# Performance work log

Measured on AMD Instinct MI355X. Metric: run time of the kernel, lower is better.

## Reference

```python
import jax, jax.numpy as jnp
import numpy as np
from jax import lax

DIM = 256
POS = 32
RATIO = 4
LN_EPS = 1e-5


def _layernorm(x, g, b):
    m = x.mean(-1, keepdims=True)
    v = ((x - m) ** 2).mean(-1, keepdims=True)
    return (x - m) * lax.rsqrt(v + LN_EPS) * g + b


def _pos_embed(pos, h, w):
    # pos: [1, C, POS, POS] -> bilinear (align_corners=False / half-pixel) -> [1, h*w, C]
    p = jax.image.resize(pos, (1, pos.shape[1], h, w), method='bilinear')
    return p.transpose(0, 2, 3, 1).reshape(1, h * w, pos.shape[1])


def _scan_branch(u, ln_g, ln_b, Wf, bf, Ww, bw, Wo, bo):
    # u: [B, N, C]. Pooled LN context -> concat gates -> gated linear recurrence.
    c = _layernorm(u.mean(1), ln_g, ln_b)                       # [B, C]
    z = jnp.concatenate([u, jnp.broadcast_to(c[:, None, :], u.shape)], -1)
    d = jax.nn.softplus(z @ Wf + bf)
    g = jax.nn.sigmoid(z @ Ww + bw)
    o = jax.nn.sigmoid(z @ Wo + bo)
    a = jnp.exp(-d)
    b = (1.0 - a) * (g * u)

    def step(s, t):
        a_t, b_t, o_t, u_t = t
        s = a_t * s + b_t
        return s, o_t * s + (1.0 - o_t) * u_t

    xs = tuple(jnp.swapaxes(v, 0, 1) for v in (a, b, o, u))     # [N, B, C]
    s0 = jnp.zeros((u.shape[0], u.shape[2]), u.dtype)
    _, y = lax.scan(step, s0, xs)
    return jnp.swapaxes(y, 0, 1)                                # [B, N, C]


def setup_inputs() -> dict:
    key = jax.random.key(0)
    ks = jax.random.split(key, 32)
    d = DIM

    def W(k, i, o, s=0.02):
        return (jax.random.normal(k, (i, o), jnp.float32) * s)

    inp = {
        'x': jax.random.normal(ks[0], (8, d, 64, 64), jnp.float32),
        'Wt': W(ks[1], d, d), 'bt': jnp.zeros((d,), jnp.float32),
        'pos_fine': jax.random.normal(ks[2], (1, d, POS, POS), jnp.float32) * 0.02,
        'pos_glob': jax.random.normal(ks[3], (1, d, POS, POS), jnp.float32) * 0.02,
        'ln_g': jnp.ones((d,), jnp.float32), 'ln_b': jnp.zeros((d,), jnp.float32),
        'Wf': W(ks[4], 2 * d, d), 'bf': jnp.zeros((d,), jnp.float32),
        'Ww': W(ks[5], 2 * d, d), 'bw': jnp.zeros((d,), jnp.float32),
        'Wo': W(ks[6], 2 * d, d), 'bo': jnp.zeros((d,), jnp.float32),
        'Wr': W(ks[7], 3 * d, d), 'br': jnp.zeros((d,), jnp.float32),
        'Wgi': W(ks[8], 3 * d, d), 'bgi': jnp.zeros((d,), jnp.float32),
        'dw_w': jax.random.normal(ks[9], (d, 1, 3, 3), jnp.float32) * 0.1,
        'dw_b': jnp.zeros((d,), jnp.float32),
        'Wl': W(ks[10], d, d), 'bl': jnp.zeros((d,), jnp.float32),
        'Wlf': W(ks[11], 2 * d, d), 'blf': jnp.zeros((d,), jnp.float32),
        'Wout': W(ks[12], d, d), 'bout': jnp.zeros((d,), jnp.float32),
    }
    return inp


def reference(x, Wt, bt, pos_fine, pos_glob, ln_g, ln_b, Wf, bf, Ww, bw, Wo, bo,
              Wr, br, Wgi, bgi, dw_w, dw_b, Wl, bl, Wlf, blf, Wout, bout):
    bsz, c, h, w = x.shape
    gate_params = (ln_g, ln_b, Wf, bf, Ww, bw, Wo, bo)

    # fine sequence: token proj + interpolated learnable pos
    seq = x.transpose(0, 2, 3, 1).reshape(bsz, h * w, c)
    u = seq @ Wt + bt + _pos_embed(pos_fine, h, w)

    # bidirectional gated scan
    y_f = _scan_branch(u, *gate_params)
    y_b = jnp.flip(_scan_branch(jnp.flip(u, 1), *gate_params), 1)
    rho = jax.nn.sigmoid(jnp.concatenate([u, y_f, y_b], -1) @ Wr + br)
    y = rho * y_f + (1.0 - rho) * y_b

    # global branch: exact avg pool (H,W divisible by RATIO) -> scan -> upsample
    gh, gw = h // RATIO, w // RATIO
    x_g = x.reshape(bsz, c, gh, RATIO, gw, RATIO).mean((3, 5))
    seq_g = x_g.transpose(0, 2, 3, 1).reshape(bsz, gh * gw, c)
    u_g = seq_g @ Wt + bt + _pos_embed(pos_glob, gh, gw)
    y_g = _scan_branch(u_g, *gate_params)
    y_g_map = y_g.reshape(bsz, gh, gw, c).transpose(0, 3, 1, 2)
    y_g_up = jax.image.resize(y_g_map, (bsz, c, h, w), method='bilinear')
    y_g_seq = y_g_up.transpose(0, 2, 3, 1).reshape(bsz, h * w, c)

    lam = jax.nn.sigmoid(jnp.concatenate([y, y_g_seq, u], -1) @ Wgi + bgi)
    z = y + lam * y_g_seq

    # local depthwise conv branch
    v_map = lax.conv_general_dilated(x, dw_w, (1, 1), 'SAME',
                                     feature_group_count=c) + dw_b[None, :, None, None]
    v = v_map.transpose(0, 2, 3, 1).reshape(bsz, h * w, c) @ Wl + bl
    eta = jax.nn.sigmoid(jnp.concatenate([v, z], -1) @ Wlf + blf)
    u_out = eta * v + (1.0 - eta) * z

    # 1x1 conv output proj + residual
    out_map = (u_out @ Wout + bout).reshape(bsz, h, w, c).transpose(0, 3, 1, 2)
    return x + out_map
```

## Files before the change

### kernel.cpp

```cpp
#include <hip/hip_runtime.h>
#include <cstddef>

#define B_  8
#define C_  256
#define H_  64
#define W_  64
#define HW_ 4096
#define NG_ 256

typedef unsigned short u16;
typedef __attribute__((ext_vector_type(8))) short short8;
typedef __attribute__((ext_vector_type(4))) float f32x4;

__device__ __forceinline__ float sigm(float v) { return 1.f / (1.f + expf(-v)); }

__device__ __forceinline__ u16 f2bf(float f) {
    union { float f; unsigned u; } x; x.f = f;
    unsigned r = x.u + 0x7fff + ((x.u >> 16) & 1);
    return (u16)(r >> 16);
}
__device__ __forceinline__ float bf2f(u16 h) {
    union { unsigned u; float f; } x; x.u = ((unsigned)h) << 16;
    return x.f;
}

__global__ __launch_bounds__(256) void prepw_k(
    const float* __restrict__ Wt, const float* __restrict__ Wf, const float* __restrict__ Ww,
    const float* __restrict__ Wo, const float* __restrict__ Wr, const float* __restrict__ Wgi,
    const float* __restrict__ Wl, const float* __restrict__ Wlf, const float* __restrict__ Wout,
    u16* __restrict__ Wpre)
{
    int s = blockIdx.z;
    const float* Wsrc; int rowoff = 0;
    switch (s) {
        case 0: Wsrc = Wt; break;
        case 1: Wsrc = Wf; break;
        case 2: Wsrc = Ww; break;
        case 3: Wsrc = Wo; break;
        case 4: case 5: case 6: Wsrc = Wr;  rowoff = (s - 4) * 256; break;
        case 7: case 8: case 9: Wsrc = Wgi; rowoff = (s - 7) * 256; break;
        case 10: Wsrc = Wl; break;
        case 11: case 12: Wsrc = Wlf; rowoff = (s - 11) * 256; break;
        default: Wsrc = Wout; break;
    }
    __shared__ float t[32][33];
    int k0 = blockIdx.y * 32, n0 = blockIdx.x * 32;
    int tx = threadIdx.x, ty = threadIdx.y;
#pragma unroll
    for (int i = 0; i < 32; i += 8)
        t[ty + i][tx] = Wsrc[(size_t)(rowoff + k0 + ty + i) * 256 + n0 + tx];
    __syncthreads();
    u16* op = Wpre + (size_t)s * 65536;
#pragma unroll
    for (int i = 0; i < 32; i += 8)
        op[(size_t)(n0 + ty + i) * 256 + k0 + tx] = f2bf(t[tx][ty + i]);
}

#define LDK 72
__global__ __launch_bounds__(256, 4) void gemm_bf16(
    const u16* __restrict__ A0, const u16* __restrict__ A1, const u16* __restrict__ A2,
    int nseg, const u16* __restrict__ Wpre, const float* __restrict__ bias,
    const float* __restrict__ pos, const float* __restrict__ aux0,
    const u16* __restrict__ auxb0, const u16* __restrict__ auxb1,
    float* __restrict__ out, u16* __restrict__ out2, int NTOK, int mode)
{
    __shared__ u16 Asm[64 * LDK];
    __shared__ u16 Bsm[128 * LDK];
    const int tid = threadIdx.x;
    const int lane = tid & 63, wave = tid >> 6;
    const int wm = wave & 1, wn = wave >> 1;
    const int m0 = blockIdx.x * 64, n0 = blockIdx.y * 128;
    const int l15 = lane & 15, lq = lane >> 4;

    f32x4 acc[2][4] = {};

    const int rowA = tid >> 2, kA = (tid & 3) * 16;
    const int rowB = tid >> 1, kB = (tid & 1) * 32;

    for (int seg = 0; seg < nseg; ++seg) {
        const u16* __restrict__ A = (seg == 0) ? A0 : ((seg == 1) ? A1 : A2);
        const u16* arow = A + (size_t)(m0 + rowA) * 256 + kA;
        const u16* wrow = Wpre + (size_t)seg * 65536 + (size_t)(n0 + rowB) * 256 + kB;

        for (int k0 = 0; k0 < 256; k0 += 64) {
            *(short8*)(&Asm[rowA * LDK + kA])     = *(const short8*)(arow + k0);
            *(short8*)(&Asm[rowA * LDK + kA + 8]) = *(const short8*)(arow + k0 + 8);
#pragma unroll
            for (int c = 0; c < 4; ++c)
                *(short8*)(&Bsm[rowB * LDK + kB + c * 8]) =
                    *(const short8*)(wrow + k0 + c * 8);
            __syncthreads();

#pragma unroll
            for (int ks = 0; ks < 2; ++ks) {
                short8 af[2], bfr[4];
#pragma unroll
                for (int i = 0; i < 2; ++i)
                    af[i] = *(const short8*)(&Asm[(wm * 32 + i * 16 + l15) * LDK + ks * 32 + lq * 8]);
#pragma unroll
                for (int j = 0; j < 4; ++j)
                    bfr[j] = *(const short8*)(&Bsm[(wn * 64 + j * 16 + l15) * LDK + ks * 32 + lq * 8]);
#pragma unroll
                for (int i = 0; i < 2; ++i)
#pragma unroll
                    for (int j = 0; j < 4; ++j)
                        acc[i][j] = __builtin_amdgcn_mfma_f32_16x16x32_bf16(
                            af[i], bfr[j], acc[i][j], 0, 0, 0);
            }
            __syncthreads();
        }
    }

#pragma unroll
    for (int i = 0; i < 2; ++i) {
        int mbase = m0 + wm * 32 + i * 16 + lq * 4;
#pragma unroll
        for (int j = 0; j < 4; ++j) {
            int n = n0 + wn * 64 + j * 16 + l15;
            if (mode == 9) {
                int b9 = mbase >> 12, hw = mbase & 4095;
                size_t oi = ((size_t)b9 * 256 + n) * 4096 + hw;
                float bn = bias[n];
                float4 xr = *(const float4*)(aux0 + oi);
                float4 res;
                res.x = xr.x + acc[i][j][0] + bn;
                res.y = xr.y + acc[i][j][1] + bn;
                res.z = xr.z + acc[i][j][2] + bn;
                res.w = xr.w + acc[i][j][3] + bn;
                *(float4*)(out + oi) = res;
                continue;
            }
            float bn = bias[n];
#pragma unroll
            for (int r = 0; r < 4; ++r) {
                int m = mbase + r;
                size_t idx = (size_t)m * 256 + n;
                float D = acc[i][j][r] + bn;
                if (mode == 1) {
                    float v = D + pos[(size_t)(m % NTOK) * 256 + n];
                    out[idx] = v; out2[idx] = f2bf(v);
                } else if (mode == 10) {
                    float v = D + pos[(size_t)(m % NTOK) * 256 + n];
                    out2[idx] = f2bf(v);
                } else if (mode == 11) {
                    float r_ = sigm(D);
                    out2[idx] = f2bf(r_ * bf2f(auxb0[idx]) + (1.f - r_) * bf2f(auxb1[idx]));
                } else if (mode == 6) {
                    float l = sigm(D);
                    out2[idx] = f2bf(bf2f(auxb1[idx]) + l * bf2f(auxb0[idx]));
                } else if (mode == 7) {
                    out2[idx] = f2bf(D);
                } else {
                    float e = sigm(D);
                    out2[idx] = f2bf(e * bf2f(auxb0[idx]) + (1.f - e) * bf2f(auxb1[idx]));
                }
            }
        }
    }
}

__global__ __launch_bounds__(256, 4) void gemm_gates3(
    const u16* __restrict__ A0, const u16* __restrict__ Wg, const float* __restrict__ cf,
    const u16* __restrict__ ubf, float* __restrict__ aF, float* __restrict__ bbF,
    u16* __restrict__ obf, int NTOK)
{
    __shared__ u16 Asm[64 * LDK];
    __shared__ u16 Bsm[3][64 * LDK];
    const int tid = threadIdx.x;
    const int lane = tid & 63, wave = tid >> 6;
    const int wm = wave & 1, wn = wave >> 1;
    const int m0 = blockIdx.x * 64, n0 = blockIdx.y * 64;
    const int l15 = lane & 15, lq = lane >> 4;

    f32x4 acc[3][2][2] = {};

    const int rowA = tid >> 2, kA = (tid & 3) * 16;
    const u16* arow = A0 + (size_t)(m0 + rowA) * 256 + kA;
    const u16* wrow = Wg + (size_t)(n0 + rowA) * 256 + kA;

    for (int k0 = 0; k0 < 256; k0 += 64) {
        *(short8*)(&Asm[rowA * LDK + kA])     = *(const short8*)(arow + k0);
        *(short8*)(&Asm[rowA * LDK + kA + 8]) = *(const short8*)(arow + k0 + 8);
#pragma unroll
        for (int ws = 0; ws < 3; ++ws) {
            const u16* wr = wrow + (size_t)ws * 65536 + k0;
            *(short8*)(&Bsm[ws][rowA * LDK + kA])     = *(const short8*)(wr);
            *(short8*)(&Bsm[ws][rowA * LDK + kA + 8]) = *(const short8*)(wr + 8);
        }
        __syncthreads();
#pragma unroll
        for (int ks = 0; ks < 2; ++ks) {
            short8 af[2];
#pragma unroll
            for (int i = 0; i < 2; ++i)
                af[i] = *(const short8*)(&Asm[(wm * 32 + i * 16 + l15) * LDK + ks * 32 + lq * 8]);
#pragma unroll
            for (int ws = 0; ws < 3; ++ws) {
                short8 bfr[2];
#pragma unroll
                for (int j = 0; j < 2; ++j)
                    bfr[j] = *(const short8*)(&Bsm[ws][(wn * 32 + j * 16 + l15) * LDK + ks * 32 + lq * 8]);
#pragma unroll
                for (int i = 0; i < 2; ++i)
#pragma unroll
                    for (int j = 0; j < 2; ++j)
                        acc[ws][i][j] = __builtin_amdgcn_mfma_f32_16x16x32_bf16(
                            af[i], bfr[j], acc[ws][i][j], 0, 0, 0);
            }
        }
        __syncthreads();
    }

#pragma unroll
    for (int i = 0; i < 2; ++i) {
        int mbase = m0 + wm * 32 + i * 16 + lq * 4;
        int bt_ = mbase / NTOK;
#pragma unroll
        for (int j = 0; j < 2; ++j) {
            int n = n0 + wn * 32 + j * 16 + l15;
            float cD = cf[((size_t)0 * B_ + bt_) * C_ + n];
            float cW = cf[((size_t)1 * B_ + bt_) * C_ + n];
            float cO = cf[((size_t)2 * B_ + bt_) * C_ + n];
#pragma unroll
            for (int r = 0; r < 4; ++r) {
                size_t idx = (size_t)(mbase + r) * 256 + n;
                float a_ = sigm(-(acc[0][i][j][r] + cD));
                float g_ = sigm(acc[1][i][j][r] + cW);
                float o_ = sigm(acc[2][i][j][r] + cO);
                float u_ = bf2f(ubf[idx]);
                aF[idx]  = a_;
                bbF[idx] = (1.f - a_) * g_ * u_;
                obf[idx] = f2bf(o_);
            }
        }
    }
}

__global__ __launch_bounds__(256) void transpose_bf_k(const float* __restrict__ in,
                                                      u16* __restrict__ outb)
{
    __shared__ float t[32][33];
    int b = blockIdx.z;
    int r0 = blockIdx.y * 32, c0 = blockIdx.x * 32;
    int tx = threadIdx.x, ty = threadIdx.y;
    const float* ip = in + (size_t)b * HW_ * C_;
    u16* op = outb + (size_t)b * HW_ * C_;
#pragma unroll
    for (int k = 0; k < 32; k += 8)
        t[ty + k][tx] = ip[(size_t)(r0 + ty + k) * HW_ + c0 + tx];
    __syncthreads();
#pragma unroll
    for (int k = 0; k < 32; k += 8)
        op[(size_t)(c0 + ty + k) * C_ + r0 + tx] = f2bf(t[tx][ty + k]);
}

__global__ __launch_bounds__(256) void dwconvt3_k(const float* __restrict__ x,
                                                  const float* __restrict__ dww,
                                                  const float* __restrict__ dwb,
                                                  u16* __restrict__ vseq)
{
    __shared__ float sx[32 * 384];
    __shared__ float sw[32 * 9];
    __shared__ float sb[32];
    const int t = threadIdx.x;
    const int l   = (blockIdx.x & 7) * 128 + (blockIdx.x >> 3);
    const int hch = l & 15;
    const int chb = (l >> 4) & 7;
    const int b   = l >> 7;
    const int r0 = chb * 32, h0 = hch * 4;

    for (int p = t; p < 288; p += 256) sw[p] = dww[(size_t)(r0 + p / 9) * 9 + p % 9];
    if (t < 32) sb[t] = dwb[r0 + t];

    const float* xb = x + (size_t)(b * 256 + r0) * 4096;
#pragma unroll
    for (int j = 0; j < 12; ++j) {
        int seg = j * 256 + t;
        int ch  = seg / 96;
        int r4  = seg - ch * 96;
        int rr  = r4 >> 4;
        int w4  = (r4 & 15) * 4;
        int hh  = h0 - 1 + rr;
        float4 v = make_float4(0.f, 0.f, 0.f, 0.f);
        if (hh >= 0 && hh <= 63)
            v = *(const float4*)(xb + (size_t)ch * 4096 + hh * 64 + w4);
        *(float4*)(&sx[seg * 4]) = v;
    }
    __syncthreads();

    const int w = t & 63, chq = t >> 6;
    float res[4][8];
#pragma unroll
    for (int i = 0; i < 8; ++i) {
        const int ch = chq * 8 + i;
        const float* cw = &sw[ch * 9];
        const float* bp = &sx[ch * 384 + w];
        float aa[4];
        aa[0] = aa[1] = aa[2] = aa[3] = sb[ch];
#pragma unroll
        for (int rr = 0; rr < 6; ++rr) {
            const float* rp = bp + rr * 64;
            float cc = rp[0];
            float lf = (w > 0)  ? rp[-1] : 0.f;
            float rt = (w < 63) ? rp[1]  : 0.f;
            if (rr < 4)            aa[rr]     += lf * cw[0] + cc * cw[1] + rt * cw[2];
            if (rr >= 1 && rr < 5) aa[rr - 1] += lf * cw[3] + cc * cw[4] + rt * cw[5];
            if (rr >= 2)           aa[rr - 2] += lf * cw[6] + cc * cw[7] + rt * cw[8];
        }
#pragma unroll
        for (int r = 0; r < 4; ++r) res[r][i] = aa[r];
    }

    size_t obase = ((size_t)b * HW_ + (size_t)(h0 * 64 + w)) * 256 + r0 + chq * 8;
#pragma unroll
    for (int r = 0; r < 4; ++r) {
        short8 v;
#pragma unroll
        for (int i = 0; i < 8; ++i) v[i] = (short)f2bf(res[r][i]);
        *(short8*)(vseq + obase + (size_t)r * 64 * 256) = v;
    }
}

__global__ __launch_bounds__(256) void pool_k(const float* __restrict__ x, u16* __restrict__ seqg)
{
    int b = blockIdx.x, c = blockIdx.y, ghw = threadIdx.x;
    int gh = ghw >> 4, gw = ghw & 15;
    const float* xp = x + ((size_t)b * C_ + c) * HW_;
    float s = 0.f;
#pragma unroll
    for (int dy = 0; dy < 4; ++dy)
#pragma unroll
        for (int dx = 0; dx < 4; ++dx)
            s += xp[(gh * 4 + dy) * W_ + gw * 4 + dx];
    seqg[((size_t)b * NG_ + ghw) * C_ + c] = f2bf(s * (1.f / 16.f));
}

__global__ __launch_bounds__(256) void posfine_k(const float* __restrict__ pf, float* __restrict__ posF)
{
    int hw = blockIdx.x, c = threadIdx.x;
    int h = hw >> 6, w = hw & 63;
    float fy = h * 0.5f - 0.25f, fx = w * 0.5f - 0.25f;
    int y0 = (int)floorf(fy); float wy = fy - (float)y0;
    int x0 = (int)floorf(fx); float wx = fx - (float)x0;
    int y0c = min(max(y0, 0), 31), y1c = min(max(y0 + 1, 0), 31);
    int x0c = min(max(x0, 0), 31), x1c = min(max(x0 + 1, 0), 31);
    const float* p = pf + (size_t)c * 1024;
    float v = (1.f - wy) * ((1.f - wx) * p[y0c * 32 + x0c] + wx * p[y0c * 32 + x1c])
            +        wy  * ((1.f - wx) * p[y1c * 32 + x0c] + wx * p[y1c * 32 + x1c]);
    posF[(size_t)hw * C_ + c] = v;
}

__global__ __launch_bounds__(256) void posglob_k(const float* __restrict__ pg, float* __restrict__ posG)
{
    int ghw = blockIdx.x, c = threadIdx.x;
    int gh = ghw >> 4, gw = ghw & 15;
    const float wt[4] = {0.125f, 0.375f, 0.375f, 0.125f};
    float wy[4], wx[4]; int jy[4], jx[4];
    float sy = 0.f, sx = 0.f;
#pragma unroll
    for (int k = 0; k < 4; ++k) {
        jy[k] = 2 * gh - 1 + k; jx[k] = 2 * gw - 1 + k;
        wy[k] = (jy[k] >= 0 && jy[k] < 32) ? wt[k] : 0.f; sy += wy[k];
        wx[k] = (jx[k] >= 0 && jx[k] < 32) ? wt[k] : 0.f; sx += wx[k];
    }
    const float* p = pg + (size_t)c * 1024;
    float acc = 0.f;
#pragma unroll
    for (int ky = 0; ky < 4; ++ky) {
        if (wy[ky] == 0.f) continue;
        float row = 0.f;
#pragma unroll
        for (int kx = 0; kx < 4; ++kx)
            if (wx[kx] != 0.f) row += wx[kx] * p[jy[ky] * 32 + jx[kx]];
        acc += wy[ky] * row;
    }
    posG[(size_t)ghw * C_ + c] = acc / (sy * sx);
}

__global__ __launch_bounds__(256) void upsample_k(const float* __restrict__ yg, u16* __restrict__ ygs)
{
    int b = blockIdx.x >> 12, hw = blockIdx.x & 4095, c = threadIdx.x;
    int h = hw >> 6, w = hw & 63;
    float fy = h * 0.25f - 0.375f, fx = w * 0.25f - 0.375f;
    int y0 = (int)floorf(fy); float wy = fy - (float)y0;
    int x0 = (int)floorf(fx); float wx = fx - (float)x0;
    int y0c = min(max(y0, 0), 15), y1c = min(max(y0 + 1, 0), 15);
    int x0c = min(max(x0, 0), 15), x1c = min(max(x0 + 1, 0), 15);
    const float* p = yg + (size_t)b * NG_ * C_ + c;
    float v = (1.f - wy) * ((1.f - wx) * p[(y0c * 16 + x0c) * C_] + wx * p[(y0c * 16 + x1c) * C_])
            +        wy  * ((1.f - wx) * p[(y1c * 16 + x0c) * C_] + wx * p[(y1c * 16 + x1c) * C_]);
    ygs[((size_t)b * HW_ + hw) * C_ + c] = f2bf(v);
}

__global__ __launch_bounds__(256) void meanpart_k(const float* __restrict__ u, float* __restrict__ part,
                                                  int Ntok, int chunkLen)
{
    int b = blockIdx.x, s = blockIdx.y, c = threadIdx.x;
    float acc = 0.f;
    for (int i = 0; i < chunkLen; ++i) {
        int t = s * chunkLen + i;
        acc += u[((size_t)b * Ntok + t) * C_ + c];
    }
    part[((size_t)b * gridDim.y + s) * C_ + c] = acc;
}

__global__ __launch_bounds__(256) void meanpart_bf_k(const u16* __restrict__ u, float* __restrict__ part,
                                                     int Ntok, int chunkLen)
{
    int b = blockIdx.x, s = blockIdx.y, c = threadIdx.x;
    float acc = 0.f;
    for (int i = 0; i < chunkLen; ++i) {
        int t = s * chunkLen + i;
        acc += bf2f(u[((size_t)b * Ntok + t) * C_ + c]);
    }
    part[((size_t)b * gridDim.y + s) * C_ + c] = acc;
}

__global__ __launch_bounds__(256) void ln_k(const float* __restrict__ part, int S, float invN,
                                            const float* __restrict__ g, const float* __restrict__ bta,
                                            float* __restrict__ cout)
{
    __shared__ float red[256];
    int c = threadIdx.x, b = blockIdx.x;
    float v = 0.f;
    for (int s = 0; s < S; ++s) v += part[((size_t)b * S + s) * C_ + c];
    v *= invN;
    red[c] = v; __syncthreads();
    for (int st = 128; st > 0; st >>= 1) { if (c < st) red[c] += red[c + st]; __syncthreads(); }
    float m = red[0] * (1.f / 256.f);
    __syncthreads();
    float d = v - m;
    red[c] = d * d; __syncthreads();
    for (int st = 128; st > 0; st >>= 1) { if (c < st) red[c] += red[c + st]; __syncthreads(); }
    float var = red[0] * (1.f / 256.f);
    cout[(size_t)b * C_ + c] = d * rsqrtf(var + 1e-5f) * g[c] + bta[c];
}

__global__ __launch_bounds__(256) void gatebias_k(const float* __restrict__ cvec,
    const float* __restrict__ Wf, const float* __restrict__ bf,
    const float* __restrict__ Ww, const float* __restrict__ bw,
    const float* __restrict__ Wo, const float* __restrict__ bo,
    float* __restrict__ outb)
{
    int n = threadIdx.x, b = blockIdx.x, gate = blockIdx.y;
    const float* Wm = (gate == 0) ? Wf : ((gate == 1) ? Ww : Wo);
    const float* bi = (gate == 0) ? bf : ((gate == 1) ? bw : bo);
    __shared__ float cs[256];
    cs[n] = cvec[(size_t)b * C_ + n];
    __syncthreads();
    float acc = bi[n];
    for (int k = 0; k < 256; ++k)
        acc += cs[k] * Wm[(size_t)(256 + k) * C_ + n];
    outb[((size_t)gate * B_ + b) * C_ + n] = acc;
}

__global__ __launch_bounds__(256) void scan_p1b(
    const float* __restrict__ a, const float* __restrict__ bb,
    float* __restrict__ AbF, float* __restrict__ BbF,
    float* __restrict__ AbB, float* __restrict__ BbB,
    int Ntok, int nchunk, int both)
{
    int c = threadIdx.x;
    int ch = blockIdx.x % nchunk;
    int b = blockIdx.x / nchunk;
    int CL = Ntok / nchunk;
    size_t base = ((size_t)b * Ntok + (size_t)ch * CL) * C_ + c;
    float sA = 1.f, sB = 0.f;
    for (int i = 0; i < CL; ++i) {
        float av = a[base + (size_t)i * C_];
        sB = av * sB + bb[base + (size_t)i * C_];
        sA *= av;
    }
    size_t o = ((size_t)b * nchunk + ch) * C_ + c;
    AbF[o] = sA; BbF[o] = sB;
    if (both) {
        sA = 1.f; sB = 0.f;
        for (int i = CL - 1; i >= 0; --i) {
            float av = a[base + (size_t)i * C_];
            sB = av * sB + bb[base + (size_t)i * C_];
            sA *= av;
        }
        size_t ob = ((size_t)b * nchunk + (nchunk - 1 - ch)) * C_ + c;
        AbB[ob] = sA; BbB[ob] = sB;
    }
}

__global__ __launch_bounds__(512) void scan_p2c(
    const float* __restrict__ AbF, const float* __restrict__ BbF, float* __restrict__ SbF,
    const float* __restrict__ AbB, const float* __restrict__ BbB, float* __restrict__ SbB,
    int nchunk, int both)
{
    const int c = threadIdx.x & 255, half = threadIdx.x >> 8, b = blockIdx.x;
    if (half && !both) return;
    const float* __restrict__ Ap = half ? AbB : AbF;
    const float* __restrict__ Bp = half ? BbB : BbF;
    float* __restrict__       Sp = half ? SbB : SbF;
    const size_t base = (size_t)b * nchunk * C_ + c;
    float a0[8], b0[8], a1[8], b1[8];
#pragma unroll
    for (int j = 0; j < 8; ++j) {
        a0[j] = Ap[base + (size_t)j * C_];
        b0[j] = Bp[base + (size_t)j * C_];
    }
    float s = 0.f;
    const int nb = nchunk >> 3;
    for (int t = 0; t < nb; ++t) {
        const size_t nbase = base + (size_t)(t + 1) * 8 * C_;
        if (t + 1 < nb) {
#pragma unroll
            for (int j = 0; j < 8; ++j) {
                a1[j] = Ap[nbase + (size_t)j * C_];
                b1[j] = Bp[nbase + (size_t)j * C_];
            }
        }
        const size_t cbase = base + (size_t)t * 8 * C_;
#pragma unroll
        for (int j = 0; j < 8; ++j) {
            Sp[cbase + (size_t)j * C_] = s;
            s = a0[j] * s + b0[j];
        }
#pragma unroll
        for (int j = 0; j < 8; ++j) { a0[j] = a1[j]; b0[j] = b1[j]; }
    }
}

__global__ __launch_bounds__(256) void scan_p3b(
    const float* __restrict__ a, const float* __restrict__ bb,
    const u16* __restrict__ obf, const u16* __restrict__ ubf,
    const float* __restrict__ SbF, const float* __restrict__ SbB,
    float* __restrict__ yout, u16* __restrict__ ybfF, u16* __restrict__ ybfB,
    int Ntok, int nchunk, int both)
{
    int c = threadIdx.x;
    int ch = blockIdx.x % nchunk;
    int b = blockIdx.x / nchunk;
    int CL = Ntok / nchunk;
    size_t base = ((size_t)b * Ntok + (size_t)ch * CL) * C_ + c;
    float s = SbF[((size_t)b * nchunk + ch) * C_ + c];
    for (int i = 0; i < CL; ++i) {
        size_t idx = base + (size_t)i * C_;
        float av = a[idx];
        s = av * s + bb[idx];
        float ov = bf2f(obf[idx]);
        float y = ov * s + (1.f - ov) * bf2f(ubf[idx]);
        if (yout) yout[idx] = y;
        if (ybfF) ybfF[idx] = f2bf(y);
    }
    if (both) {
        float sb = SbB[((size_t)b * nchunk + (nchunk - 1 - ch)) * C_ + c];
        for (int i = CL - 1; i >= 0; --i) {
            size_t idx = base + (size_t)i * C_;
            float av = a[idx];
            sb = av * sb + bb[idx];
            float ov = bf2f(obf[idx]);
            ybfB[idx] = f2bf(ov * sb + (1.f - ov) * bf2f(ubf[idx]));
        }
    }
}

extern "C" void kernel_launch(void* const* d_in, const int* in_sizes, int n_in,
                              void* d_out, int out_size, void* d_ws, size_t ws_size,
                              hipStream_t stream)
{
    const float* x        = (const float*)d_in[0];
    const float* Wt       = (const float*)d_in[1];
    const float* bt       = (const float*)d_in[2];
    const float* pos_fine = (const float*)d_in[3];
    const float* pos_glob = (const float*)d_in[4];
    const float* ln_g     = (const float*)d_in[5];
    const float* ln_b     = (const float*)d_in[6];
    const float* Wf       = (const float*)d_in[7];
    const float* bf       = (const float*)d_in[8];
    const float* Ww       = (const float*)d_in[9];
    const float* bw       = (const float*)d_in[10];
    const float* Wo       = (const float*)d_in[11];
    const float* bo       = (const float*)d_in[12];
    const float* Wr       = (const float*)d_in[13];
    const float* br       = (const float*)d_in[14];
    const float* Wgi      = (const float*)d_in[15];
    const float* bgi      = (const float*)d_in[16];
    const float* dww      = (const float*)d_in[17];
    const float* dwb      = (const float*)d_in[18];
    const float* Wl       = (const float*)d_in[19];
    const float* bl       = (const float*)d_in[20];
    const float* Wlf      = (const float*)d_in[21];
    const float* blf      = (const float*)d_in[22];
    const float* Wout     = (const float*)d_in[23];
    const float* bout     = (const float*)d_in[24];
    float* out = (float*)d_out;

    float* w = (float*)d_ws;
    const size_t BNC = (size_t)B_ * HW_ * C_;
    float* bu  = w + 0 * BNC;
    float* ba  = w + 1 * BNC;
    float* bbb = w + 2 * BNC;
    float* bo_ = w + 3 * BNC;
    u16* bf1 = (u16*)(w + 4 * BNC);
    u16* bf2 = bf1 + BNC;
    u16* bf3 = bf2 + BNC;
    u16* bf4 = bf3 + BNC;
    u16* bf5 = bf4 + BNC;
    float* ext = w + 4 * BNC + 5 * (BNC / 2);
    float* posF = ext;  ext += (size_t)HW_ * C_;
    float* posG = ext;  ext += (size_t)NG_ * C_;
    float* part = ext;  ext += (size_t)B_ * 32 * C_;
    float* cln  = ext;  ext += (size_t)B_ * C_;
    float* cf   = ext;  ext += (size_t)3 * B_ * C_;
    float* ug   = ext;  ext += (size_t)B_ * NG_ * C_;
    float* ag   = ext;  ext += (size_t)B_ * NG_ * C_;
    float* bbg  = ext;  ext += (size_t)B_ * NG_ * C_;
    float* ygt  = ext;  ext += (size_t)B_ * NG_ * C_;
    u16* seqg_bf = (u16*)ext;  ext += (size_t)B_ * NG_ * C_ / 2;
    u16* ug_bf   = (u16*)ext;  ext += (size_t)B_ * NG_ * C_ / 2;
    u16* og_bf   = (u16*)ext;  ext += (size_t)B_ * NG_ * C_ / 2;
    u16* Wpre    = (u16*)ext;
    const size_t CHS = (size_t)B_ * 256 * C_;
    float* chAF = bu + 0 * CHS;
    float* chBF = bu + 1 * CHS;
    float* chSF = bu + 2 * CHS;
    float* chAB = bu + 3 * CHS;
    float* chBB = bu + 4 * CHS;
    float* chSB = bu + 5 * CHS;
    u16* obf    = (u16*)bo_;

    const dim3 blk256(256);
    const dim3 blkT(32, 8);
    const dim3 gBig(B_ * HW_ / 64, 2);
    const dim3 gSml(B_ * NG_ / 64, 2);
    const dim3 gGateF(B_ * HW_ / 64, 4);
    const dim3 gGateG(B_ * NG_ / 64, 4);
    const size_t WS = 65536;
    const int NCH_F = 256;
    const int NCH_G = 16;
    const float *F0 = nullptr; const u16 *U0 = nullptr;
    float *FW = nullptr; u16 *UW = nullptr;

    prepw_k<<<dim3(8, 8, 14), blkT, 0, stream>>>(Wt, Wf, Ww, Wo, Wr, Wgi, Wl, Wlf, Wout, Wpre);

    transpose_bf_k<<<dim3(HW_ / 32, C_ / 32, B_), blkT, 0, stream>>>(x, bf1);
    posfine_k<<<HW_, blk256, 0, stream>>>(pos_fine, posF);
    gemm_bf16<<<gBig, blk256, 0, stream>>>(bf1, U0, U0, 1, Wpre + 0 * WS, bt,
        posF, F0, U0, U0, FW, bf2, HW_, 10);

    pool_k<<<dim3(B_, C_), blk256, 0, stream>>>(x, seqg_bf);
    posglob_k<<<NG_, blk256, 0, stream>>>(pos_glob, posG);
    gemm_bf16<<<gSml, blk256, 0, stream>>>(seqg_bf, U0, U0, 1, Wpre + 0 * WS, bt,
        posG, F0, U0, U0, ug, ug_bf, NG_, 1);
    meanpart_k<<<dim3(B_, 8), blk256, 0, stream>>>(ug, part, NG_, 32);
    ln_k<<<B_, blk256, 0, stream>>>(part, 8, 1.f / NG_, ln_g, ln_b, cln);
    gatebias_k<<<dim3(B_, 3), blk256, 0, stream>>>(cln, Wf, bf, Ww, bw, Wo, bo, cf);
    gemm_gates3<<<gGateG, blk256, 0, stream>>>(ug_bf, Wpre + 1 * WS, cf, ug_bf,
        ag, bbg, og_bf, NG_);
    scan_p1b<<<B_ * NCH_G, blk256, 0, stream>>>(ag, bbg, chAF, chBF, FW, FW, NG_, NCH_G, 0);
    scan_p2c<<<B_, dim3(512), 0, stream>>>(chAF, chBF, chSF, F0, F0, FW, NCH_G, 0);
    scan_p3b<<<B_ * NCH_G, blk256, 0, stream>>>(ag, bbg, og_bf, ug_bf, chSF, F0,
        ygt, UW, UW, NG_, NCH_G, 0);
    upsample_k<<<B_ * HW_, blk256, 0, stream>>>(ygt, bf5);

    meanpart_bf_k<<<dim3(B_, 32), blk256, 0, stream>>>(bf2, part, HW_, 128);
    ln_k<<<B_, blk256, 0, stream>>>(part, 32, 1.f / HW_, ln_g, ln_b, cln);
    gatebias_k<<<dim3(B_, 3), blk256, 0, stream>>>(cln, Wf, bf, Ww, bw, Wo, bo, cf);
    gemm_gates3<<<gGateF, blk256, 0, stream>>>(bf2, Wpre + 1 * WS, cf, bf2,
        ba, bbb, obf, HW_);
    scan_p1b<<<B_ * NCH_F, blk256, 0, stream>>>(ba, bbb, chAF, chBF, chAB, chBB, HW_, NCH_F, 1);
    scan_p2c<<<B_, dim3(512), 0, stream>>>(chAF, chBF, chSF, chAB, chBB, chSB, NCH_F, 1);
    scan_p3b<<<B_ * NCH_F, blk256, 0, stream>>>(ba, bbb, obf, bf2, chSF, chSB,
        FW, bf1, bf3, HW_, NCH_F, 1);

    gemm_bf16<<<gBig, blk256, 0, stream>>>(bf2, bf1, bf3, 3, Wpre + 4 * WS, br,
        F0, F0, bf1, bf3, FW, bf4, HW_, 11);

    gemm_bf16<<<gBig, blk256, 0, stream>>>(bf4, bf5, bf2, 3, Wpre + 7 * WS, bgi,
        F0, F0, bf5, bf4, FW, bf1, HW_, 6);

    dwconvt3_k<<<dim3(1024), blk256, 0, stream>>>(x, dww, dwb, bf3);
    gemm_bf16<<<gBig, blk256, 0, stream>>>(bf3, U0, U0, 1, Wpre + 10 * WS, bl,
        F0, F0, U0, U0, FW, bf2, HW_, 7);
    gemm_bf16<<<gBig, blk256, 0, stream>>>(bf2, bf1, U0, 2, Wpre + 11 * WS, blf,
        F0, F0, bf2, bf1, FW, bf3, HW_, 8);

    gemm_bf16<<<gBig, blk256, 0, stream>>>(bf3, U0, U0, 1, Wpre + 13 * WS, bout,
        F0, x, U0, U0, out, UW, HW_, 9);
}
```

Measured before the change: 596.0 us.

## Retile bf16 GEMM to 128x256 blocks with A loaded directly to registers

```diff
diff --git a/kernel.cpp b/kernel.cpp
--- a/kernel.cpp
+++ b/kernel.cpp
@@ -57,66 +57,81 @@
 }
 
 #define LDK 72
-__global__ __launch_bounds__(256, 4) void gemm_bf16(
+__global__ __launch_bounds__(256, 1) void gemm_bf16(
     const u16* __restrict__ A0, const u16* __restrict__ A1, const u16* __restrict__ A2,
     int nseg, const u16* __restrict__ Wpre, const float* __restrict__ bias,
     const float* __restrict__ pos, const float* __restrict__ aux0,
     const u16* __restrict__ auxb0, const u16* __restrict__ auxb1,
     float* __restrict__ out, u16* __restrict__ out2, int NTOK, int mode)
 {
-    __shared__ u16 Asm[64 * LDK];
-    __shared__ u16 Bsm[128 * LDK];
+    __shared__ u16 Bsm[256 * LDK];
     const int tid = threadIdx.x;
     const int lane = tid & 63, wave = tid >> 6;
     const int wm = wave & 1, wn = wave >> 1;
-    const int m0 = blockIdx.x * 64, n0 = blockIdx.y * 128;
+    const int m0 = blockIdx.x * 128;
     const int l15 = lane & 15, lq = lane >> 4;
 
-    f32x4 acc[2][4] = {};
-
-    const int rowA = tid >> 2, kA = (tid & 3) * 16;
-    const int rowB = tid >> 1, kB = (tid & 1) * 32;
-
-    for (int seg = 0; seg < nseg; ++seg) {
-        const u16* __restrict__ A = (seg == 0) ? A0 : ((seg == 1) ? A1 : A2);
-        const u16* arow = A + (size_t)(m0 + rowA) * 256 + kA;
-        const u16* wrow = Wpre + (size_t)seg * 65536 + (size_t)(n0 + rowB) * 256 + kB;
-
-        for (int k0 = 0; k0 < 256; k0 += 64) {
-            *(short8*)(&Asm[rowA * LDK + kA])     = *(const short8*)(arow + k0);
-            *(short8*)(&Asm[rowA * LDK + kA + 8]) = *(const short8*)(arow + k0 + 8);
-#pragma unroll
-            for (int c = 0; c < 4; ++c)
-                *(short8*)(&Bsm[rowB * LDK + kB + c * 8]) =
-                    *(const short8*)(wrow + k0 + c * 8);
-            __syncthreads();
-
-#pragma unroll
-            for (int ks = 0; ks < 2; ++ks) {
-                short8 af[2], bfr[4];
-#pragma unroll
-                for (int i = 0; i < 2; ++i)
-                    af[i] = *(const short8*)(&Asm[(wm * 32 + i * 16 + l15) * LDK + ks * 32 + lq * 8]);
-#pragma unroll
-                for (int j = 0; j < 4; ++j)
-                    bfr[j] = *(const short8*)(&Bsm[(wn * 64 + j * 16 + l15) * LDK + ks * 32 + lq * 8]);
-#pragma unroll
-                for (int i = 0; i < 2; ++i)
-#pragma unroll
-                    for (int j = 0; j < 4; ++j)
-                        acc[i][j] = __builtin_amdgcn_mfma_f32_16x16x32_bf16(
-                            af[i], bfr[j], acc[i][j], 0, 0, 0);
-            }
-            __syncthreads();
-        }
-    }
-
-#pragma unroll
-    for (int i = 0; i < 2; ++i) {
-        int mbase = m0 + wm * 32 + i * 16 + lq * 4;
-#pragma unroll
-        for (int j = 0; j < 4; ++j) {
-            int n = n0 + wn * 64 + j * 16 + l15;
+    f32x4 acc[4][8] = {};
+
+    short8 breg[8];
+    const u16* wrow = Wpre + (size_t)tid * 256;
+#pragma unroll
+    for (int c = 0; c < 8; ++c)
+        breg[c] = *(const short8*)(wrow + c * 8);
+
+    const int nq = nseg * 4;
+    for (int q = 0; q < nq; ++q) {
+        const int seg = q >> 2, k0 = (q & 3) << 6;
+        const u16* __restrict__ Aq = (seg == 0) ? A0 : ((seg == 1) ? A1 : A2);
+        const u16* arow = Aq + (size_t)(m0 + wm * 64 + l15) * 256 + k0 + lq * 8;
+
+        __syncthreads();
+#pragma unroll
+        for (int c = 0; c < 8; ++c)
+            *(short8*)(&Bsm[tid * LDK + c * 8]) = breg[c];
+        if (q + 1 < nq) {
+            const u16* wnext = Wpre + (size_t)((q + 1) >> 2) * 65536
+                             + (size_t)(((q + 1) & 3) << 6) + (size_t)tid * 256;
+#pragma unroll
+            for (int c = 0; c < 8; ++c)
+                breg[c] = *(const short8*)(wnext + c * 8);
+        }
+        short8 af0[4], af1[4];
+#pragma unroll
+        for (int i = 0; i < 4; ++i)
+            af0[i] = *(const short8*)(arow + (size_t)i * 16 * 256);
+        __syncthreads();
+#pragma unroll
+        for (int i = 0; i < 4; ++i)
+            af1[i] = *(const short8*)(arow + (size_t)i * 16 * 256 + 32);
+
+        short8 bfr[8];
+#pragma unroll
+        for (int j = 0; j < 8; ++j)
+            bfr[j] = *(const short8*)(&Bsm[(wn * 128 + j * 16 + l15) * LDK + lq * 8]);
+#pragma unroll
+        for (int i = 0; i < 4; ++i)
+#pragma unroll
+            for (int j = 0; j < 8; ++j)
+                acc[i][j] = __builtin_amdgcn_mfma_f32_16x16x32_bf16(
+                    af0[i], bfr[j], acc[i][j], 0, 0, 0);
+#pragma unroll
+        for (int j = 0; j < 8; ++j)
+            bfr[j] = *(const short8*)(&Bsm[(wn * 128 + j * 16 + l15) * LDK + 32 + lq * 8]);
+#pragma unroll
+        for (int i = 0; i < 4; ++i)
+#pragma unroll
+            for (int j = 0; j < 8; ++j)
+                acc[i][j] = __builtin_amdgcn_mfma_f32_16x16x32_bf16(
+                    af1[i], bfr[j], acc[i][j], 0, 0, 0);
+    }
+
+#pragma unroll
+    for (int i = 0; i < 4; ++i) {
+        int mbase = m0 + wm * 64 + i * 16 + lq * 4;
+#pragma unroll
+        for (int j = 0; j < 8; ++j) {
+            int n = wn * 128 + j * 16 + l15;
             if (mode == 9) {
                 int b9 = mbase >> 12, hw = mbase & 4095;
                 size_t oi = ((size_t)b9 * 256 + n) * 4096 + hw;
@@ -165,7 +180,7 @@
     u16* __restrict__ obf, int NTOK)
 {
     __shared__ u16 Asm[64 * LDK];
-    __shared__ u16 Bsm[3][64 * LDK];
+    __shared__ u16 Bsm3[3][64 * LDK];
     const int tid = threadIdx.x;
     const int lane = tid & 63, wave = tid >> 6;
     const int wm = wave & 1, wn = wave >> 1;
@@ -184,8 +199,8 @@
 #pragma unroll
         for (int ws = 0; ws < 3; ++ws) {
             const u16* wr = wrow + (size_t)ws * 65536 + k0;
-            *(short8*)(&Bsm[ws][rowA * LDK + kA])     = *(const short8*)(wr);
-            *(short8*)(&Bsm[ws][rowA * LDK + kA + 8]) = *(const short8*)(wr + 8);
+            *(short8*)(&Bsm3[ws][rowA * LDK + kA])     = *(const short8*)(wr);
+            *(short8*)(&Bsm3[ws][rowA * LDK + kA + 8]) = *(const short8*)(wr + 8);
         }
         __syncthreads();
 #pragma unroll
@@ -199,7 +214,7 @@
                 short8 bfr[2];
 #pragma unroll
                 for (int j = 0; j < 2; ++j)
-                    bfr[j] = *(const short8*)(&Bsm[ws][(wn * 32 + j * 16 + l15) * LDK + ks * 32 + lq * 8]);
+                    bfr[j] = *(const short8*)(&Bsm3[ws][(wn * 32 + j * 16 + l15) * LDK + ks * 32 + lq * 8]);
 #pragma unroll
                 for (int i = 0; i < 2; ++i)
 #pragma unroll
@@ -625,8 +640,8 @@
 
     const dim3 blk256(256);
     const dim3 blkT(32, 8);
-    const dim3 gBig(B_ * HW_ / 64, 2);
-    const dim3 gSml(B_ * NG_ / 64, 2);
+    const dim3 gBig(B_ * HW_ / 128);
+    const dim3 gSml(B_ * NG_ / 128);
     const dim3 gGateF(B_ * HW_ / 64, 4);
     const dim3 gGateG(B_ * NG_ / 64, 4);
     const size_t WS = 65536;
```

New measurement: 1.863 ms. 213% more time.

## Load GEMM tiles via global_load_lds into fragment-ordered LDS with 128x128 tiles

Applied to the files above, without the earlier changes.

```diff
diff --git a/kernel.cpp b/kernel.cpp
--- a/kernel.cpp
+++ b/kernel.cpp
@@ -22,6 +22,12 @@
 __device__ __forceinline__ float bf2f(u16 h) {
     union { unsigned u; float f; } x; x.u = ((unsigned)h) << 16;
     return x.f;
+}
+
+__device__ __forceinline__ void gl_lds16(const u16* g, u16* l) {
+    __builtin_amdgcn_global_load_lds(
+        (const __attribute__((address_space(1))) unsigned int*)g,
+        (__attribute__((address_space(3))) unsigned int*)l, 16, 0, 0);
 }
 
 __global__ __launch_bounds__(256) void prepw_k(
@@ -56,64 +62,61 @@
         op[(size_t)(n0 + ty + i) * 256 + k0 + tx] = f2bf(t[tx][ty + i]);
 }
 
-#define LDK 72
-__global__ __launch_bounds__(256, 4) void gemm_bf16(
+__global__ __launch_bounds__(256, 2) void gemm_bf16(
     const u16* __restrict__ A0, const u16* __restrict__ A1, const u16* __restrict__ A2,
     int nseg, const u16* __restrict__ Wpre, const float* __restrict__ bias,
     const float* __restrict__ pos, const float* __restrict__ aux0,
     const u16* __restrict__ auxb0, const u16* __restrict__ auxb1,
     float* __restrict__ out, u16* __restrict__ out2, int NTOK, int mode)
 {
-    __shared__ u16 Asm[64 * LDK];
-    __shared__ u16 Bsm[128 * LDK];
+    __shared__ u16 Asm[16 * 512];
+    __shared__ u16 Bsm[16 * 512];
     const int tid = threadIdx.x;
-    const int lane = tid & 63, wave = tid >> 6;
-    const int wm = wave & 1, wn = wave >> 1;
-    const int m0 = blockIdx.x * 64, n0 = blockIdx.y * 128;
+    const int lane = tid & 63, wv = tid >> 6;
+    const int wm = wv & 1, wn = wv >> 1;
+    const int m0 = blockIdx.x * 128, n0 = blockIdx.y * 128;
     const int l15 = lane & 15, lq = lane >> 4;
 
-    f32x4 acc[2][4] = {};
-
-    const int rowA = tid >> 2, kA = (tid & 3) * 16;
-    const int rowB = tid >> 1, kB = (tid & 1) * 32;
-
-    for (int seg = 0; seg < nseg; ++seg) {
-        const u16* __restrict__ A = (seg == 0) ? A0 : ((seg == 1) ? A1 : A2);
-        const u16* arow = A + (size_t)(m0 + rowA) * 256 + kA;
-        const u16* wrow = Wpre + (size_t)seg * 65536 + (size_t)(n0 + rowB) * 256 + kB;
-
-        for (int k0 = 0; k0 < 256; k0 += 64) {
-            *(short8*)(&Asm[rowA * LDK + kA])     = *(const short8*)(arow + k0);
-            *(short8*)(&Asm[rowA * LDK + kA + 8]) = *(const short8*)(arow + k0 + 8);
-#pragma unroll
-            for (int c = 0; c < 4; ++c)
-                *(short8*)(&Bsm[rowB * LDK + kB + c * 8]) =
-                    *(const short8*)(wrow + k0 + c * 8);
-            __syncthreads();
-
-#pragma unroll
-            for (int ks = 0; ks < 2; ++ks) {
-                short8 af[2], bfr[4];
-#pragma unroll
-                for (int i = 0; i < 2; ++i)
-                    af[i] = *(const short8*)(&Asm[(wm * 32 + i * 16 + l15) * LDK + ks * 32 + lq * 8]);
+    f32x4 acc[4][4] = {};
+
+    const int nq = nseg * 4;
+    for (int q = 0; q < nq; ++q) {
+        const int seg = q >> 2, k0 = (q & 3) << 6;
+        const u16* __restrict__ Aq = (seg == 0) ? A0 : ((seg == 1) ? A1 : A2);
+        const u16* __restrict__ Wq = Wpre + (size_t)seg * 65536;
+
+        __syncthreads();
+#pragma unroll
+        for (int c = 0; c < 4; ++c) {
+            const int tile = wv * 4 + c;
+            const int rset = (tile >> 3) * 64 + ((tile >> 1) & 3) * 16 + l15;
+            const int kset = k0 + (tile & 1) * 32 + lq * 8;
+            gl_lds16(Aq + (size_t)(m0 + rset) * 256 + kset, &Asm[tile * 512 + lane * 8]);
+            gl_lds16(Wq + (size_t)(n0 + rset) * 256 + kset, &Bsm[tile * 512 + lane * 8]);
+        }
+        __syncthreads();
+
+#pragma unroll
+        for (int ks = 0; ks < 2; ++ks) {
+            short8 af[4], bfr[4];
+#pragma unroll
+            for (int i = 0; i < 4; ++i)
+                af[i] = *(const short8*)(&Asm[(wm * 8 + i * 2 + ks) * 512 + lane * 8]);
+#pragma unroll
+            for (int j = 0; j < 4; ++j)
+                bfr[j] = *(const short8*)(&Bsm[(wn * 8 + j * 2 + ks) * 512 + lane * 8]);
+#pragma unroll
+            for (int i = 0; i < 4; ++i)
 #pragma unroll
                 for (int j = 0; j < 4; ++j)
-                    bfr[j] = *(const short8*)(&Bsm[(wn * 64 + j * 16 + l15) * LDK + ks * 32 + lq * 8]);
-#pragma unroll
-                for (int i = 0; i < 2; ++i)
-#pragma unroll
-                    for (int j = 0; j < 4; ++j)
-                        acc[i][j] = __builtin_amdgcn_mfma_f32_16x16x32_bf16(
-                            af[i], bfr[j], acc[i][j], 0, 0, 0);
-            }
-            __syncthreads();
-        }
-    }
-
-#pragma unroll
-    for (int i = 0; i < 2; ++i) {
-        int mbase = m0 + wm * 32 + i * 16 + lq * 4;
+                    acc[i][j] = __builtin_amdgcn_mfma_f32_16x16x32_bf16(
+                        af[i], bfr[j], acc[i][j], 0, 0, 0);
+        }
+    }
+
+#pragma unroll
+    for (int i = 0; i < 4; ++i) {
+        int mbase = m0 + wm * 64 + i * 16 + lq * 4;
 #pragma unroll
         for (int j = 0; j < 4; ++j) {
             int n = n0 + wn * 64 + j * 16 + l15;
@@ -159,13 +162,14 @@
     }
 }
 
+#define LDK 72
 __global__ __launch_bounds__(256, 4) void gemm_gates3(
     const u16* __restrict__ A0, const u16* __restrict__ Wg, const float* __restrict__ cf,
     const u16* __restrict__ ubf, float* __restrict__ aF, float* __restrict__ bbF,
     u16* __restrict__ obf, int NTOK)
 {
     __shared__ u16 Asm[64 * LDK];
-    __shared__ u16 Bsm[3][64 * LDK];
+    __shared__ u16 Bsm3[3][64 * LDK];
     const int tid = threadIdx.x;
     const int lane = tid & 63, wave = tid >> 6;
     const int wm = wave & 1, wn = wave >> 1;
@@ -184,8 +188,8 @@
 #pragma unroll
         for (int ws = 0; ws < 3; ++ws) {
             const u16* wr = wrow + (size_t)ws * 65536 + k0;
-            *(short8*)(&Bsm[ws][rowA * LDK + kA])     = *(const short8*)(wr);
-            *(short8*)(&Bsm[ws][rowA * LDK + kA + 8]) = *(const short8*)(wr + 8);
+            *(short8*)(&Bsm3[ws][rowA * LDK + kA])     = *(const short8*)(wr);
+            *(short8*)(&Bsm3[ws][rowA * LDK + kA + 8]) = *(const short8*)(wr + 8);
         }
         __syncthreads();
 #pragma unroll
@@ -199,7 +203,7 @@
                 short8 bfr[2];
 #pragma unroll
                 for (int j = 0; j < 2; ++j)
-                    bfr[j] = *(const short8*)(&Bsm[ws][(wn * 32 + j * 16 + l15) * LDK + ks * 32 + lq * 8]);
+                    bfr[j] = *(const short8*)(&Bsm3[ws][(wn * 32 + j * 16 + l15) * LDK + ks * 32 + lq * 8]);
 #pragma unroll
                 for (int i = 0; i < 2; ++i)
 #pragma unroll
@@ -625,8 +629,8 @@
 
     const dim3 blk256(256);
     const dim3 blkT(32, 8);
-    const dim3 gBig(B_ * HW_ / 64, 2);
-    const dim3 gSml(B_ * NG_ / 64, 2);
+    const dim3 gBig(B_ * HW_ / 128, 2);
+    const dim3 gSml(B_ * NG_ / 128, 2);
     const dim3 gGateF(B_ * HW_ / 64, 4);
     const dim3 gGateG(B_ * NG_ / 64, 4);
     const size_t WS = 65536;
```

Measured after the change: 700.2 us. 1.17x slower.

## Register-prefetch next K tile and XOR-swizzle LDS in gemm_bf16

Applied to the files above, without the earlier changes.

```diff
diff --git a/kernel.cpp b/kernel.cpp
--- a/kernel.cpp
+++ b/kernel.cpp
@@ -56,7 +56,8 @@
         op[(size_t)(n0 + ty + i) * 256 + k0 + tx] = f2bf(t[tx][ty + i]);
 }
 
-#define LDK 72
+#define SWZ(row, qoff) ((row) * 128 + ((qoff) ^ (((row) & 7) << 4)))
+
 __global__ __launch_bounds__(256, 4) void gemm_bf16(
     const u16* __restrict__ A0, const u16* __restrict__ A1, const u16* __restrict__ A2,
     int nseg, const u16* __restrict__ Wpre, const float* __restrict__ bias,
@@ -64,8 +65,8 @@
     const u16* __restrict__ auxb0, const u16* __restrict__ auxb1,
     float* __restrict__ out, u16* __restrict__ out2, int NTOK, int mode)
 {
-    __shared__ u16 Asm[64 * LDK];
-    __shared__ u16 Bsm[128 * LDK];
+    __shared__ u16 Asm[64 * 64];
+    __shared__ u16 Bsm[128 * 64];
     const int tid = threadIdx.x;
     const int lane = tid & 63, wave = tid >> 6;
     const int wm = wave & 1, wn = wave >> 1;
@@ -74,40 +75,57 @@
 
     f32x4 acc[2][4] = {};
 
-    const int rowA = tid >> 2, kA = (tid & 3) * 16;
-    const int rowB = tid >> 1, kB = (tid & 1) * 32;
-
-    for (int seg = 0; seg < nseg; ++seg) {
-        const u16* __restrict__ A = (seg == 0) ? A0 : ((seg == 1) ? A1 : A2);
-        const u16* arow = A + (size_t)(m0 + rowA) * 256 + kA;
-        const u16* wrow = Wpre + (size_t)seg * 65536 + (size_t)(n0 + rowB) * 256 + kB;
-
-        for (int k0 = 0; k0 < 256; k0 += 64) {
-            *(short8*)(&Asm[rowA * LDK + kA])     = *(const short8*)(arow + k0);
-            *(short8*)(&Asm[rowA * LDK + kA + 8]) = *(const short8*)(arow + k0 + 8);
-#pragma unroll
-            for (int c = 0; c < 4; ++c)
-                *(short8*)(&Bsm[rowB * LDK + kB + c * 8]) =
-                    *(const short8*)(wrow + k0 + c * 8);
-            __syncthreads();
-
-#pragma unroll
-            for (int ks = 0; ks < 2; ++ks) {
-                short8 af[2], bfr[4];
-#pragma unroll
-                for (int i = 0; i < 2; ++i)
-                    af[i] = *(const short8*)(&Asm[(wm * 32 + i * 16 + l15) * LDK + ks * 32 + lq * 8]);
+    const int rowS = tid >> 3, colS = tid & 7;
+
+    short8 av[2], bv[4];
+    {
+        av[0] = *(const short8*)(A0 + (size_t)(m0 + rowS) * 256 + colS * 8);
+        av[1] = *(const short8*)(A0 + (size_t)(m0 + 32 + rowS) * 256 + colS * 8);
+#pragma unroll
+        for (int i = 0; i < 4; ++i)
+            bv[i] = *(const short8*)(Wpre + (size_t)(n0 + i * 32 + rowS) * 256 + colS * 8);
+    }
+
+    const int nq = nseg * 4;
+    for (int q = 0; q < nq; ++q) {
+        __syncthreads();
+        *(short8*)((char*)Asm + SWZ(rowS,      colS * 16)) = av[0];
+        *(short8*)((char*)Asm + SWZ(rowS + 32, colS * 16)) = av[1];
+#pragma unroll
+        for (int i = 0; i < 4; ++i)
+            *(short8*)((char*)Bsm + SWZ(i * 32 + rowS, colS * 16)) = bv[i];
+
+        if (q + 1 < nq) {
+            const int q1 = q + 1, seg = q1 >> 2, k0 = (q1 & 3) << 6;
+            const u16* __restrict__ A = (seg == 0) ? A0 : ((seg == 1) ? A1 : A2);
+            const u16* __restrict__ Wq = Wpre + (size_t)seg * 65536;
+            av[0] = *(const short8*)(A + (size_t)(m0 + rowS) * 256 + k0 + colS * 8);
+            av[1] = *(const short8*)(A + (size_t)(m0 + 32 + rowS) * 256 + k0 + colS * 8);
+#pragma unroll
+            for (int i = 0; i < 4; ++i)
+                bv[i] = *(const short8*)(Wq + (size_t)(n0 + i * 32 + rowS) * 256 + k0 + colS * 8);
+        }
+        __syncthreads();
+
+#pragma unroll
+        for (int ks = 0; ks < 2; ++ks) {
+            short8 af[2], bfr[4];
+#pragma unroll
+            for (int i = 0; i < 2; ++i) {
+                const int row = wm * 32 + i * 16 + l15;
+                af[i] = *(const short8*)((char*)Asm + SWZ(row, ks * 64 + lq * 16));
+            }
+#pragma unroll
+            for (int j = 0; j < 4; ++j) {
+                const int row = wn * 64 + j * 16 + l15;
+                bfr[j] = *(const short8*)((char*)Bsm + SWZ(row, ks * 64 + lq * 16));
+            }
+#pragma unroll
+            for (int i = 0; i < 2; ++i)
 #pragma unroll
                 for (int j = 0; j < 4; ++j)
-                    bfr[j] = *(const short8*)(&Bsm[(wn * 64 + j * 16 + l15) * LDK + ks * 32 + lq * 8]);
-#pragma unroll
-                for (int i = 0; i < 2; ++i)
-#pragma unroll
-                    for (int j = 0; j < 4; ++j)
-                        acc[i][j] = __builtin_amdgcn_mfma_f32_16x16x32_bf16(
-                            af[i], bfr[j], acc[i][j], 0, 0, 0);
-            }
-            __syncthreads();
+                    acc[i][j] = __builtin_amdgcn_mfma_f32_16x16x32_bf16(
+                        af[i], bfr[j], acc[i][j], 0, 0, 0);
         }
     }
 
@@ -159,13 +177,14 @@
     }
 }
 
+#define LDK 72
 __global__ __launch_bounds__(256, 4) void gemm_gates3(
     const u16* __restrict__ A0, const u16* __restrict__ Wg, const float* __restrict__ cf,
     const u16* __restrict__ ubf, float* __restrict__ aF, float* __restrict__ bbF,
     u16* __restrict__ obf, int NTOK)
 {
     __shared__ u16 Asm[64 * LDK];
-    __shared__ u16 Bsm[3][64 * LDK];
+    __shared__ u16 Bsm3[3][64 * LDK];
     const int tid = threadIdx.x;
     const int lane = tid & 63, wave = tid >> 6;
     const int wm = wave & 1, wn = wave >> 1;
@@ -184,8 +203,8 @@
 #pragma unroll
         for (int ws = 0; ws < 3; ++ws) {
             const u16* wr = wrow + (size_t)ws * 65536 + k0;
-            *(short8*)(&Bsm[ws][rowA * LDK + kA])     = *(const short8*)(wr);
-            *(short8*)(&Bsm[ws][rowA * LDK + kA + 8]) = *(const short8*)(wr + 8);
+            *(short8*)(&Bsm3[ws][rowA * LDK + kA])     = *(const short8*)(wr);
+            *(short8*)(&Bsm3[ws][rowA * LDK + kA + 8]) = *(const short8*)(wr + 8);
         }
         __syncthreads();
 #pragma unroll
@@ -199,7 +218,7 @@
                 short8 bfr[2];
 #pragma unroll
                 for (int j = 0; j < 2; ++j)
-                    bfr[j] = *(const short8*)(&Bsm[ws][(wn * 32 + j * 16 + l15) * LDK + ks * 32 + lq * 8]);
+                    bfr[j] = *(const short8*)(&Bsm3[ws][(wn * 32 + j * 16 + l15) * LDK + ks * 32 + lq * 8]);
 #pragma unroll
                 for (int i = 0; i < 2; ++i)
 #pragma unroll
```

New measurement: 568.4 us. 1.05x faster.
